# Kernel tuning notes

Hardware: AMD Instinct MI355X
Metric: run time of the kernel (lower is better)

## Reference

```python
import jax, jax.numpy as jnp
import numpy as np

B, T, C, H = 128, 256, 64, 128  # batch, seq_len, num_channels, hidden_size


def setup_inputs() -> dict:
    key = jax.random.key(0)
    ks = jax.random.split(key, 7)
    s = 1.0 / np.sqrt(H)  # PyTorch LSTM/Linear init bound
    x = jax.random.normal(ks[0], (B, T, C), dtype=jnp.float32)
    # Per-channel LSTM weights (input_size=1). Gate order i,f,g,o like PyTorch.
    w_ih = jax.random.uniform(ks[1], (C, 4 * H), jnp.float32, -s, s)      # [C,4H] (input is scalar)
    w_hh = jax.random.uniform(ks[2], (C, 4 * H, H), jnp.float32, -s, s)   # [C,4H,H]
    b_ih = jax.random.uniform(ks[3], (C, 4 * H), jnp.float32, -s, s)
    b_hh = jax.random.uniform(ks[4], (C, 4 * H), jnp.float32, -s, s)
    # Per-channel Linear(H, 1) head.
    w_fc = jax.random.uniform(ks[5], (C, H), jnp.float32, -s, s)
    b_fc = jax.random.uniform(ks[6], (C,), jnp.float32, -s, s)
    return {"x": x, "w_ih": w_ih, "w_hh": w_hh, "b_ih": b_ih,
            "b_hh": b_hh, "w_fc": w_fc, "b_fc": b_fc}


def reference(x, w_ih, w_hh, b_ih, b_hh, w_fc, b_fc):
    # x: [B,T,C]. All C channel-LSTMs run as one batched recurrence over [B,C].
    b = b_ih + b_hh  # [C,4H]
    xt = jnp.transpose(x, (1, 0, 2))  # [T,B,C] for scan over time
    h0 = jnp.zeros((x.shape[0], x.shape[2], w_hh.shape[-1]), x.dtype)  # [B,C,H]
    c0 = h0

    def step(carry, x_t):
        h, c = carry  # [B,C,H]
        # scalar input times per-channel input weights + recurrent GEMM
        gates = x_t[..., None] * w_ih + jnp.einsum('bch,cgh->bcg', h, w_hh) + b  # [B,C,4H]
        i, f, g, o = jnp.split(gates, 4, axis=-1)
        i = jax.nn.sigmoid(i)
        f = jax.nn.sigmoid(f)
        g = jnp.tanh(g)
        o = jax.nn.sigmoid(o)
        c_new = f * c + i * g
        h_new = o * jnp.tanh(c_new)
        return (h_new, c_new), None

    (hT, _), _ = jax.lax.scan(step, (h0, c0), xt)
    # Per-channel linear head on the last hidden state -> [B,C]
    return jnp.einsum('bch,ch->bc', hT, w_fc) + b_fc
```

## Files before the change

kernel.cpp:

```cpp
#include <hip/hip_runtime.h>
#include <hip/hip_bf16.h>

typedef __bf16 bf16_t;
typedef bf16_t bf16x8 __attribute__((ext_vector_type(8)));
typedef float f32x4 __attribute__((ext_vector_type(4)));

#define B_  128
#define T_  256
#define C_  64
#define H_  128
#define G_  512
#define BT  16
#define HS  136
#define HSZ (BT*HS)

__device__ __forceinline__ float sigmoid_fast(float z) {
    return __builtin_amdgcn_rcpf(1.0f + __builtin_amdgcn_exp2f(-1.4426950408889634f * z));
}
__device__ __forceinline__ float tanh_fast(float z) {
    return 1.0f - 2.0f * __builtin_amdgcn_rcpf(1.0f + __builtin_amdgcn_exp2f(2.8853900817779268f * z));
}

__global__ __launch_bounds__(256, 2) void lstm_fused(
    const float* __restrict__ x,
    const float* __restrict__ w_ih,
    const float* __restrict__ w_hh,
    const float* __restrict__ b_ih,
    const float* __restrict__ b_hh,
    const float* __restrict__ w_fc,
    const float* __restrict__ b_fc,
    float* __restrict__ out)
{
    const int c    = blockIdx.x & (C_ - 1);
    const int bt   = blockIdx.x >> 6;
    const int b0   = bt * BT;
    const int tid  = threadIdx.x;
    const int wid  = tid >> 6;
    const int lane = tid & 63;
    const int l16  = lane & 15;
    const int lg   = lane >> 4;

    __shared__ __align__(16) bf16_t h_lds[2 * HSZ];
    __shared__ float x_lds[BT * T_];

    for (int i = tid; i < 2 * HSZ; i += 256) h_lds[i] = (bf16_t)0.0f;
    for (int i = tid; i < BT * T_; i += 256) {
        const int bl = i >> 8, t = i & 255;
        x_lds[i] = x[(size_t)(b0 + bl) * (T_ * C_) + (size_t)t * C_ + c];
    }

    bf16x8 bw[4][2][4];
    float  bias[4][2], wih[4][2];
    #pragma unroll
    for (int q = 0; q < 4; ++q) {
        #pragma unroll
        for (int u = 0; u < 2; ++u) {
            const int n = q * 128 + wid * 32 + u * 16 + l16;
            bias[q][u] = b_ih[c * G_ + n] + b_hh[c * G_ + n];
            wih[q][u]  = w_ih[c * G_ + n];
            #pragma unroll
            for (int kk = 0; kk < 4; ++kk) {
                const int k0 = kk * 32 + lg * 8;
                const float4 wa = *(const float4*)&w_hh[((size_t)(c * G_ + n)) * H_ + k0];
                const float4 wb = *(const float4*)&w_hh[((size_t)(c * G_ + n)) * H_ + k0 + 4];
                bf16x8 f;
                f[0] = (bf16_t)wa.x; f[1] = (bf16_t)wa.y; f[2] = (bf16_t)wa.z; f[3] = (bf16_t)wa.w;
                f[4] = (bf16_t)wb.x; f[5] = (bf16_t)wb.y; f[6] = (bf16_t)wb.z; f[7] = (bf16_t)wb.w;
                bw[q][u][kk] = f;
            }
        }
    }

    float cst[2][4];
    #pragma unroll
    for (int u = 0; u < 2; ++u)
        #pragma unroll
        for (int r = 0; r < 4; ++r) cst[u][r] = 0.0f;

    __syncthreads();

    const int a_base = l16 * HS;
    const int row_l  = lg * 4;
    const int col0   = wid * 32 + l16;

    for (int t = 0; t < T_; ++t) {
        const int rd = (t & 1) * HSZ;
        const int wr = ((t + 1) & 1) * HSZ;

        bf16x8 a[4];
        #pragma unroll
        for (int kk = 0; kk < 4; ++kk)
            a[kk] = *(const bf16x8*)&h_lds[rd + a_base + kk * 32 + lg * 8];

        f32x4 accv[4][2];
        #pragma unroll
        for (int q = 0; q < 4; ++q) {
            #pragma unroll
            for (int u = 0; u < 2; ++u) {
                f32x4 acc = {0.0f, 0.0f, 0.0f, 0.0f};
                #pragma unroll
                for (int kk = 0; kk < 4; ++kk)
                    acc = __builtin_amdgcn_mfma_f32_16x16x32_bf16(a[kk], bw[q][u][kk], acc, 0, 0, 0);
                accv[q][u] = acc;
            }
        }

        float xv[4];
        #pragma unroll
        for (int r = 0; r < 4; ++r) xv[r] = x_lds[(row_l + r) * T_ + t];

        #pragma unroll
        for (int u = 0; u < 2; ++u) {
            #pragma unroll
            for (int r = 0; r < 4; ++r) {
                const float zi = accv[0][u][r] + xv[r] * wih[0][u] + bias[0][u];
                const float zf = accv[1][u][r] + xv[r] * wih[1][u] + bias[1][u];
                const float zg = accv[2][u][r] + xv[r] * wih[2][u] + bias[2][u];
                const float zo = accv[3][u][r] + xv[r] * wih[3][u] + bias[3][u];
                const float ig = sigmoid_fast(zi) * tanh_fast(zg);
                const float cn = sigmoid_fast(zf) * cst[u][r] + ig;
                cst[u][r] = cn;
                const float hn = sigmoid_fast(zo) * tanh_fast(cn);
                h_lds[wr + (row_l + r) * HS + col0 + u * 16] = (bf16_t)hn;
            }
        }
        __syncthreads();
    }

    #pragma unroll
    for (int rr = 0; rr < 4; ++rr) {
        const int row = wid * 4 + rr;
        const float h0 = (float)h_lds[row * HS + 2 * lane];
        const float h1 = (float)h_lds[row * HS + 2 * lane + 1];
        const float2 wf = *(const float2*)&w_fc[c * H_ + 2 * lane];
        float p = h0 * wf.x + h1 * wf.y;
        #pragma unroll
        for (int off = 32; off; off >>= 1) p += __shfl_xor(p, off);
        if (lane == 0) out[(size_t)(b0 + row) * C_ + c] = p + b_fc[c];
    }
}

extern "C" void kernel_launch(void* const* d_in, const int* in_sizes, int n_in,
                              void* d_out, int out_size, void* d_ws, size_t ws_size,
                              hipStream_t stream) {
    const float* x    = (const float*)d_in[0];
    const float* w_ih = (const float*)d_in[1];
    const float* w_hh = (const float*)d_in[2];
    const float* b_ih = (const float*)d_in[3];
    const float* b_hh = (const float*)d_in[4];
    const float* w_fc = (const float*)d_in[5];
    const float* b_fc = (const float*)d_in[6];
    float* out = (float*)d_out;

    dim3 grid(C_ * (B_ / BT));
    dim3 block(256);
    lstm_fused<<<grid, block, 0, stream>>>(x, w_ih, w_hh, b_ih, b_hh, w_fc, b_fc, out);
}
```

Measured before the change: 413.4 us.

## Fold input term and bias into MFMA, interleave gate columns for paired h stores

```diff
diff --git a/kernel.cpp b/kernel.cpp
--- a/kernel.cpp
+++ b/kernel.cpp
@@ -3,6 +3,7 @@
 
 typedef __bf16 bf16_t;
 typedef bf16_t bf16x8 __attribute__((ext_vector_type(8)));
+typedef bf16_t bf16x2 __attribute__((ext_vector_type(2)));
 typedef float f32x4 __attribute__((ext_vector_type(4)));
 
 #define B_  128
@@ -13,6 +14,7 @@
 #define BT  16
 #define HS  136
 #define HSZ (BT*HS)
+#define XS  257
 
 __device__ __forceinline__ float sigmoid_fast(float z) {
     return __builtin_amdgcn_rcpf(1.0f + __builtin_amdgcn_exp2f(-1.4426950408889634f * z));
@@ -20,6 +22,13 @@
 __device__ __forceinline__ float tanh_fast(float z) {
     return 1.0f - 2.0f * __builtin_amdgcn_rcpf(1.0f + __builtin_amdgcn_exp2f(2.8853900817779268f * z));
 }
+__device__ __forceinline__ uint32_t cvt_pk_bf16(float a, float b) {
+    uint32_t r;
+    asm("v_cvt_pk_bf16_f32 %0, %1, %2" : "=v"(r) : "v"(a), "v"(b));
+    return r;
+}
+
+union AFrag { bf16x8 v; uint32_t w[4]; };
 
 __global__ __launch_bounds__(256, 2) void lstm_fused(
     const float* __restrict__ x,
@@ -39,34 +48,43 @@
     const int lane = tid & 63;
     const int l16  = lane & 15;
     const int lg   = lane >> 4;
+    const bool lg0 = (lg == 0);
 
     __shared__ __align__(16) bf16_t h_lds[2 * HSZ];
-    __shared__ float x_lds[BT * T_];
+    __shared__ float x_lds[BT * XS];
 
     for (int i = tid; i < 2 * HSZ; i += 256) h_lds[i] = (bf16_t)0.0f;
     for (int i = tid; i < BT * T_; i += 256) {
         const int bl = i >> 8, t = i & 255;
-        x_lds[i] = x[(size_t)(b0 + bl) * (T_ * C_) + (size_t)t * C_ + c];
+        x_lds[bl * XS + t] = x[(size_t)(b0 + bl) * (T_ * C_) + (size_t)t * C_ + c];
     }
 
     bf16x8 bw[4][2][4];
-    float  bias[4][2], wih[4][2];
+    bf16x8 b4[4][2];
+    float  bias2[4][2];
     #pragma unroll
     for (int q = 0; q < 4; ++q) {
         #pragma unroll
         for (int u = 0; u < 2; ++u) {
-            const int n = q * 128 + wid * 32 + u * 16 + l16;
-            bias[q][u] = b_ih[c * G_ + n] + b_hh[c * G_ + n];
-            wih[q][u]  = w_ih[c * G_ + n];
+            const int n = q * 128 + wid * 32 + 2 * l16 + u;
+            bias2[q][u] = b_ih[c * G_ + n] + b_hh[c * G_ + n];
+            const float wv = w_ih[c * G_ + n];
+            const bf16_t wh = (bf16_t)wv;
+            const bf16_t wl = (bf16_t)(wv - (float)wh);
+            bf16x8 f;
+            #pragma unroll
+            for (int e = 0; e < 8; ++e) f[e] = (bf16_t)0.0f;
+            if (lg0) { f[0] = wh; f[1] = wl; f[2] = wh; }
+            b4[q][u] = f;
             #pragma unroll
             for (int kk = 0; kk < 4; ++kk) {
                 const int k0 = kk * 32 + lg * 8;
                 const float4 wa = *(const float4*)&w_hh[((size_t)(c * G_ + n)) * H_ + k0];
                 const float4 wb = *(const float4*)&w_hh[((size_t)(c * G_ + n)) * H_ + k0 + 4];
-                bf16x8 f;
-                f[0] = (bf16_t)wa.x; f[1] = (bf16_t)wa.y; f[2] = (bf16_t)wa.z; f[3] = (bf16_t)wa.w;
-                f[4] = (bf16_t)wb.x; f[5] = (bf16_t)wb.y; f[6] = (bf16_t)wb.z; f[7] = (bf16_t)wb.w;
-                bw[q][u][kk] = f;
+                bf16x8 g;
+                g[0] = (bf16_t)wa.x; g[1] = (bf16_t)wa.y; g[2] = (bf16_t)wa.z; g[3] = (bf16_t)wa.w;
+                g[4] = (bf16_t)wb.x; g[5] = (bf16_t)wb.y; g[6] = (bf16_t)wb.z; g[7] = (bf16_t)wb.w;
+                bw[q][u][kk] = g;
             }
         }
     }
@@ -81,7 +99,7 @@
 
     const int a_base = l16 * HS;
     const int row_l  = lg * 4;
-    const int col0   = wid * 32 + l16;
+    const int colp   = wid * 32 + 2 * l16;
 
     for (int t = 0; t < T_; ++t) {
         const int rd = (t & 1) * HSZ;
@@ -92,37 +110,41 @@
         for (int kk = 0; kk < 4; ++kk)
             a[kk] = *(const bf16x8*)&h_lds[rd + a_base + kk * 32 + lg * 8];
 
-        f32x4 accv[4][2];
+        const float xv = x_lds[l16 * XS + t];
+        const uint32_t p0 = cvt_pk_bf16(xv, xv);
+        const float xhf = __uint_as_float(p0 << 16);
+        const uint32_t p1 = cvt_pk_bf16(xv - xhf, 0.0f);
+        AFrag af;
+        af.w[0] = lg0 ? p0 : 0u;
+        af.w[1] = lg0 ? p1 : 0u;
+        af.w[2] = 0u; af.w[3] = 0u;
+
+        float hn2[2][4];
         #pragma unroll
-        for (int q = 0; q < 4; ++q) {
+        for (int u = 0; u < 2; ++u) {
+            f32x4 accq[4];
             #pragma unroll
-            for (int u = 0; u < 2; ++u) {
-                f32x4 acc = {0.0f, 0.0f, 0.0f, 0.0f};
+            for (int q = 0; q < 4; ++q) {
+                const float bb = bias2[q][u];
+                f32x4 acc; acc[0] = bb; acc[1] = bb; acc[2] = bb; acc[3] = bb;
                 #pragma unroll
                 for (int kk = 0; kk < 4; ++kk)
                     acc = __builtin_amdgcn_mfma_f32_16x16x32_bf16(a[kk], bw[q][u][kk], acc, 0, 0, 0);
-                accv[q][u] = acc;
+                acc = __builtin_amdgcn_mfma_f32_16x16x32_bf16(af.v, b4[q][u], acc, 0, 0, 0);
+                accq[q] = acc;
+            }
+            #pragma unroll
+            for (int r = 0; r < 4; ++r) {
+                const float ig = sigmoid_fast(accq[0][r]) * tanh_fast(accq[2][r]);
+                const float cn = sigmoid_fast(accq[1][r]) * cst[u][r] + ig;
+                cst[u][r] = cn;
+                hn2[u][r] = sigmoid_fast(accq[3][r]) * tanh_fast(cn);
             }
         }
-
-        float xv[4];
         #pragma unroll
-        for (int r = 0; r < 4; ++r) xv[r] = x_lds[(row_l + r) * T_ + t];
-
-        #pragma unroll
-        for (int u = 0; u < 2; ++u) {
-            #pragma unroll
-            for (int r = 0; r < 4; ++r) {
-                const float zi = accv[0][u][r] + xv[r] * wih[0][u] + bias[0][u];
-                const float zf = accv[1][u][r] + xv[r] * wih[1][u] + bias[1][u];
-                const float zg = accv[2][u][r] + xv[r] * wih[2][u] + bias[2][u];
-                const float zo = accv[3][u][r] + xv[r] * wih[3][u] + bias[3][u];
-                const float ig = sigmoid_fast(zi) * tanh_fast(zg);
-                const float cn = sigmoid_fast(zf) * cst[u][r] + ig;
-                cst[u][r] = cn;
-                const float hn = sigmoid_fast(zo) * tanh_fast(cn);
-                h_lds[wr + (row_l + r) * HS + col0 + u * 16] = (bf16_t)hn;
-            }
+        for (int r = 0; r < 4; ++r) {
+            bf16x2 hv; hv[0] = (bf16_t)hn2[0][r]; hv[1] = (bf16_t)hn2[1][r];
+            *(bf16x2*)&h_lds[wr + (row_l + r) * HS + colp] = hv;
         }
         __syncthreads();
     }
```

New measurement: 397.7 us. 3.8% less time.

## Use 512-thread blocks, swizzle h layout, fold bias into MFMA, fuse gate math

Applied to the files above, without the earlier changes.

```diff
diff --git a/kernel.cpp b/kernel.cpp
--- a/kernel.cpp
+++ b/kernel.cpp
@@ -5,23 +5,19 @@
 typedef bf16_t bf16x8 __attribute__((ext_vector_type(8)));
 typedef float f32x4 __attribute__((ext_vector_type(4)));
 
-#define B_  128
-#define T_  256
-#define C_  64
-#define H_  128
-#define G_  512
-#define BT  16
-#define HS  136
-#define HSZ (BT*HS)
+#define B_   128
+#define T_   256
+#define C_   64
+#define H_   128
+#define G_   512
+#define BT   16
+#define XS   20
+#define HBUF 2048
 
-__device__ __forceinline__ float sigmoid_fast(float z) {
-    return __builtin_amdgcn_rcpf(1.0f + __builtin_amdgcn_exp2f(-1.4426950408889634f * z));
-}
-__device__ __forceinline__ float tanh_fast(float z) {
-    return 1.0f - 2.0f * __builtin_amdgcn_rcpf(1.0f + __builtin_amdgcn_exp2f(2.8853900817779268f * z));
-}
+#define K1 1.4426950408889634f
+#define K2 2.8853900817779268f
 
-__global__ __launch_bounds__(256, 2) void lstm_fused(
+__global__ __launch_bounds__(512, 4) void lstm_fused(
     const float* __restrict__ x,
     const float* __restrict__ w_ih,
     const float* __restrict__ w_hh,
@@ -35,103 +31,99 @@
     const int bt   = blockIdx.x >> 6;
     const int b0   = bt * BT;
     const int tid  = threadIdx.x;
-    const int wid  = tid >> 6;
+    const int w    = tid >> 6;
     const int lane = tid & 63;
     const int l16  = lane & 15;
     const int lg   = lane >> 4;
 
-    __shared__ __align__(16) bf16_t h_lds[2 * HSZ];
-    __shared__ float x_lds[BT * T_];
+    __shared__ __align__(16) bf16_t h_lds[2 * HBUF];
+    __shared__ __align__(16) float x_lds[T_ * XS];
 
-    for (int i = tid; i < 2 * HSZ; i += 256) h_lds[i] = (bf16_t)0.0f;
-    for (int i = tid; i < BT * T_; i += 256) {
+    for (int i = tid; i < HBUF; i += 512) ((uint32_t*)h_lds)[i] = 0u;
+    for (int i = tid; i < BT * T_; i += 512) {
         const int bl = i >> 8, t = i & 255;
-        x_lds[i] = x[(size_t)(b0 + bl) * (T_ * C_) + (size_t)t * C_ + c];
+        x_lds[t * XS + bl] = x[(size_t)(b0 + bl) * (T_ * C_) + (size_t)t * C_ + c];
     }
 
-    bf16x8 bw[4][2][4];
-    float  bias[4][2], wih[4][2];
+    bf16x8 bw[4][4];
+    float  bias[4], wih[4];
     #pragma unroll
     for (int q = 0; q < 4; ++q) {
+        const int n = q * 128 + w * 16 + l16;
+        bias[q] = b_ih[c * G_ + n] + b_hh[c * G_ + n];
+        wih[q]  = w_ih[c * G_ + n];
         #pragma unroll
-        for (int u = 0; u < 2; ++u) {
-            const int n = q * 128 + wid * 32 + u * 16 + l16;
-            bias[q][u] = b_ih[c * G_ + n] + b_hh[c * G_ + n];
-            wih[q][u]  = w_ih[c * G_ + n];
-            #pragma unroll
-            for (int kk = 0; kk < 4; ++kk) {
-                const int k0 = kk * 32 + lg * 8;
-                const float4 wa = *(const float4*)&w_hh[((size_t)(c * G_ + n)) * H_ + k0];
-                const float4 wb = *(const float4*)&w_hh[((size_t)(c * G_ + n)) * H_ + k0 + 4];
-                bf16x8 f;
-                f[0] = (bf16_t)wa.x; f[1] = (bf16_t)wa.y; f[2] = (bf16_t)wa.z; f[3] = (bf16_t)wa.w;
-                f[4] = (bf16_t)wb.x; f[5] = (bf16_t)wb.y; f[6] = (bf16_t)wb.z; f[7] = (bf16_t)wb.w;
-                bw[q][u][kk] = f;
-            }
+        for (int kk = 0; kk < 4; ++kk) {
+            const int k0 = kk * 32 + lg * 8;
+            const float4 wa = *(const float4*)&w_hh[((size_t)(c * G_ + n)) * H_ + k0];
+            const float4 wb = *(const float4*)&w_hh[((size_t)(c * G_ + n)) * H_ + k0 + 4];
+            bf16x8 g;
+            g[0] = (bf16_t)wa.x; g[1] = (bf16_t)wa.y; g[2] = (bf16_t)wa.z; g[3] = (bf16_t)wa.w;
+            g[4] = (bf16_t)wb.x; g[5] = (bf16_t)wb.y; g[6] = (bf16_t)wb.z; g[7] = (bf16_t)wb.w;
+            bw[q][kk] = g;
         }
     }
 
-    float cst[2][4];
-    #pragma unroll
-    for (int u = 0; u < 2; ++u)
-        #pragma unroll
-        for (int r = 0; r < 4; ++r) cst[u][r] = 0.0f;
+    float cst[4] = {0.f, 0.f, 0.f, 0.f};
 
     __syncthreads();
 
-    const int a_base = l16 * HS;
-    const int row_l  = lg * 4;
-    const int col0   = wid * 32 + l16;
+    const int a_off  = l16 * 8;
+    const int wbase  = (w * 2 + (l16 >> 3)) * 128 + lg * 32 + (l16 & 7);
 
-    for (int t = 0; t < T_; ++t) {
-        const int rd = (t & 1) * HSZ;
-        const int wr = ((t + 1) & 1) * HSZ;
+    auto step = [&](const int RD, const int WR, const int t) {
+        const f32x4 xv = *(const f32x4*)&x_lds[t * XS + lg * 4];
 
         bf16x8 a[4];
         #pragma unroll
         for (int kk = 0; kk < 4; ++kk)
-            a[kk] = *(const bf16x8*)&h_lds[rd + a_base + kk * 32 + lg * 8];
+            a[kk] = *(const bf16x8*)&h_lds[RD + (kk * 4 + lg) * 128 + a_off];
 
-        f32x4 accv[4][2];
+        f32x4 acc[4];
         #pragma unroll
-        for (int q = 0; q < 4; ++q) {
+        for (int q = 0; q < 4; ++q)
             #pragma unroll
-            for (int u = 0; u < 2; ++u) {
-                f32x4 acc = {0.0f, 0.0f, 0.0f, 0.0f};
-                #pragma unroll
-                for (int kk = 0; kk < 4; ++kk)
-                    acc = __builtin_amdgcn_mfma_f32_16x16x32_bf16(a[kk], bw[q][u][kk], acc, 0, 0, 0);
-                accv[q][u] = acc;
-            }
-        }
-
-        float xv[4];
-        #pragma unroll
-        for (int r = 0; r < 4; ++r) xv[r] = x_lds[(row_l + r) * T_ + t];
+            for (int r = 0; r < 4; ++r)
+                acc[q][r] = fmaf(xv[r], wih[q], bias[q]);
 
         #pragma unroll
-        for (int u = 0; u < 2; ++u) {
+        for (int q = 0; q < 4; ++q)
             #pragma unroll
-            for (int r = 0; r < 4; ++r) {
-                const float zi = accv[0][u][r] + xv[r] * wih[0][u] + bias[0][u];
-                const float zf = accv[1][u][r] + xv[r] * wih[1][u] + bias[1][u];
-                const float zg = accv[2][u][r] + xv[r] * wih[2][u] + bias[2][u];
-                const float zo = accv[3][u][r] + xv[r] * wih[3][u] + bias[3][u];
-                const float ig = sigmoid_fast(zi) * tanh_fast(zg);
-                const float cn = sigmoid_fast(zf) * cst[u][r] + ig;
-                cst[u][r] = cn;
-                const float hn = sigmoid_fast(zo) * tanh_fast(cn);
-                h_lds[wr + (row_l + r) * HS + col0 + u * 16] = (bf16_t)hn;
-            }
+            for (int kk = 0; kk < 4; ++kk)
+                acc[q] = __builtin_amdgcn_mfma_f32_16x16x32_bf16(a[kk], bw[q][kk], acc[q], 0, 0, 0);
+
+        #pragma unroll
+        for (int r = 0; r < 4; ++r) {
+            const float ei = __builtin_amdgcn_exp2f(-K1 * acc[0][r]);
+            const float ef = __builtin_amdgcn_exp2f(-K1 * acc[1][r]);
+            const float eg = __builtin_amdgcn_exp2f( K2 * acc[2][r]);
+            const float eo = __builtin_amdgcn_exp2f(-K1 * acc[3][r]);
+            const float A  = 1.f + ei, D = 1.f + ef, Bb = 1.f + eg, O = 1.f + eo;
+            const float AB = A * Bb;
+            const float r1 = __builtin_amdgcn_rcpf(D * AB);
+            const float cn = fmaf(D, eg - 1.f, cst[r] * AB) * r1;
+            cst[r] = cn;
+            float m2 = K2 * cn;
+            m2 = fminf(fmaxf(m2, -60.f), 60.f);
+            const float ec = __builtin_amdgcn_exp2f(m2);
+            const float r2 = __builtin_amdgcn_rcpf(O * (1.f + ec));
+            const float hv = (ec - 1.f) * r2;
+            h_lds[WR + wbase + r * 8] = (bf16_t)hv;
         }
         __syncthreads();
+    };
+
+    for (int t = 0; t < T_; t += 2) {
+        step(0, HBUF, t);
+        step(HBUF, 0, t + 1);
     }
 
     #pragma unroll
-    for (int rr = 0; rr < 4; ++rr) {
-        const int row = wid * 4 + rr;
-        const float h0 = (float)h_lds[row * HS + 2 * lane];
-        const float h1 = (float)h_lds[row * HS + 2 * lane + 1];
+    for (int rr = 0; rr < 2; ++rr) {
+        const int row = w * 2 + rr;
+        const int eaddr = (lane >> 2) * 128 + row * 8 + (lane & 3) * 2;
+        const float h0 = (float)h_lds[eaddr];
+        const float h1 = (float)h_lds[eaddr + 1];
         const float2 wf = *(const float2*)&w_fc[c * H_ + 2 * lane];
         float p = h0 * wf.x + h1 * wf.y;
         #pragma unroll
@@ -153,6 +145,6 @@
     float* out = (float*)d_out;
 
     dim3 grid(C_ * (B_ / BT));
-    dim3 block(256);
+    dim3 block(512);
     lstm_fused<<<grid, block, 0, stream>>>(x, w_ih, w_hh, b_ih, b_hh, w_fc, b_fc, out);
 }
```

New measurement: 387.6 us. 6.2% less time.
